# Performance work log

Hardware: AMD Instinct MI355X
Metric: run time of the kernel (lower is better)

Reference implementation:

```python
import jax, jax.numpy as jnp
import numpy as np


def setup_inputs() -> dict:
    key = jax.random.key(0)
    k1, k2 = jax.random.split(key)
    x = jax.random.normal(k1, (16, 256, 128, 128), dtype=jnp.float32)
    conv_w = jax.random.normal(k2, (1, 2, 3, 3), dtype=jnp.float32) * 0.1
    return {"x": x, "conv_w": conv_w}


def reference(x, conv_w):
    # x: [B, C, H, W]; channel-wise mean and max -> [B, 2, H, W]
    x_avg = jnp.mean(x, axis=1, keepdims=True)
    x_max = jnp.max(x, axis=1, keepdims=True)
    feat = jnp.concatenate([x_avg, x_max], axis=1)
    # 3x3 conv, stride 1, padding 1, no bias; NCHW / OIHW
    y = jax.lax.conv_general_dilated(
        feat, conv_w,
        window_strides=(1, 1), padding=((1, 1), (1, 1)),
        dimension_numbers=("NCHW", "OIHW", "NCHW"))
    return jax.nn.sigmoid(y)  # [B, 1, H, W]
```

## Files before the change

kernel.cpp:

```cpp
#include <hip/hip_runtime.h>
#include <math.h>

#define B 16
#define C 256
#define H 128
#define W 128
#define HW (H * W)
#define HW4 (HW / 4)

typedef float vfloat4 __attribute__((ext_vector_type(4)));

__global__ __launch_bounds__(256, 4) void reduce_mean_max(
    const float* __restrict__ x, float* __restrict__ feat) {
  const int t    = threadIdx.x;
  const int lane = t & 63;
  const int cq   = t >> 6;
  const int chunk = blockIdx.x * 64 + lane;
  const int b    = chunk >> 12;
  const int s4   = chunk & (HW4 - 1);

  const vfloat4* xp = (const vfloat4*)x + (size_t)(b * C + cq * 64) * HW4 + s4;

  vfloat4 sum = (vfloat4)(0.f);
  vfloat4 mx  = (vfloat4)(-INFINITY);
#pragma unroll 8
  for (int c = 0; c < 64; ++c) {
    vfloat4 v = xp[(size_t)c * HW4];
    sum += v;
    mx.x = fmaxf(mx.x, v.x); mx.y = fmaxf(mx.y, v.y);
    mx.z = fmaxf(mx.z, v.z); mx.w = fmaxf(mx.w, v.w);
  }

  __shared__ vfloat4 s_sum[4][64];
  __shared__ vfloat4 s_max[4][64];
  s_sum[cq][lane] = sum;
  s_max[cq][lane] = mx;
  __syncthreads();

  if (cq == 0) {
    vfloat4 a = s_sum[0][lane], b1 = s_sum[1][lane],
            c2 = s_sum[2][lane], d = s_sum[3][lane];
    const float inv = 1.0f / (float)C;
    vfloat4 mean = (a + b1 + c2 + d) * inv;
    ((vfloat4*)feat)[(size_t)(b * 2) * HW4 + s4] = mean;
  } else if (cq == 1) {
    vfloat4 a = s_max[0][lane], b1 = s_max[1][lane],
            c2 = s_max[2][lane], d = s_max[3][lane];
    vfloat4 m;
    m.x = fmaxf(fmaxf(a.x, b1.x), fmaxf(c2.x, d.x));
    m.y = fmaxf(fmaxf(a.y, b1.y), fmaxf(c2.y, d.y));
    m.z = fmaxf(fmaxf(a.z, b1.z), fmaxf(c2.z, d.z));
    m.w = fmaxf(fmaxf(a.w, b1.w), fmaxf(c2.w, d.w));
    ((vfloat4*)feat)[(size_t)(b * 2 + 1) * HW4 + s4] = m;
  }
}

__global__ __launch_bounds__(256) void conv3x3_sigmoid(
    const float* __restrict__ feat, const float* __restrict__ wgt,
    float* __restrict__ out) {
  __shared__ float sw[18];
  if (threadIdx.x < 18) sw[threadIdx.x] = wgt[threadIdx.x];
  __syncthreads();

  const int idx = blockIdx.x * 256 + threadIdx.x;
  const int b = idx >> 14;
  const int s = idx & (HW - 1);
  const int h = s >> 7;
  const int w = s & (W - 1);

  float acc = 0.f;
#pragma unroll
  for (int ci = 0; ci < 2; ++ci) {
    const float* f  = feat + (size_t)(b * 2 + ci) * HW;
    const float* kw = sw + ci * 9;
#pragma unroll
    for (int dh = -1; dh <= 1; ++dh) {
      const int hh = h + dh;
      if (hh < 0 || hh >= H) continue;
      const float* row = f + hh * W;
#pragma unroll
      for (int dw = -1; dw <= 1; ++dw) {
        const int ww = w + dw;
        if (ww < 0 || ww >= W) continue;
        acc += row[ww] * kw[(dh + 1) * 3 + (dw + 1)];
      }
    }
  }
  out[idx] = 1.f / (1.f + __expf(-acc));
}

extern "C" void kernel_launch(void* const* d_in, const int* in_sizes, int n_in,
                              void* d_out, int out_size, void* d_ws, size_t ws_size,
                              hipStream_t stream) {
  const float* x   = (const float*)d_in[0];
  const float* wgt = (const float*)d_in[1];
  float* out  = (float*)d_out;
  float* feat = (float*)d_ws;

  reduce_mean_max<<<1024, 256, 0, stream>>>(x, feat);
  conv3x3_sigmoid<<<1024, 256, 0, stream>>>(feat, wgt, out);
}
```

Measured before the change: 356.7 us.

## Restructure channel reduction into larger blocks with per-thread multi-chunk accumulation

The mean/max reduction now uses 256 blocks of 512 threads. Each wave handles 32 channels and each thread accumulates four separate spatial vectors, giving more independent loads in flight per thread. Partial results are combined across 8 waves through a shared buffer in two passes (sum, then max). This trades occupancy and block count for per-thread memory-level parallelism, and leaves exactly one block per CU.

```diff
diff --git a/kernel.cpp b/kernel.cpp
--- a/kernel.cpp
+++ b/kernel.cpp
@@ -10,48 +10,69 @@
 
 typedef float vfloat4 __attribute__((ext_vector_type(4)));
 
-__global__ __launch_bounds__(256, 4) void reduce_mean_max(
+__global__ __launch_bounds__(512) void reduce_mean_max(
     const float* __restrict__ x, float* __restrict__ feat) {
   const int t    = threadIdx.x;
   const int lane = t & 63;
-  const int cq   = t >> 6;
-  const int chunk = blockIdx.x * 64 + lane;
-  const int b    = chunk >> 12;
-  const int s4   = chunk & (HW4 - 1);
+  const int wv   = t >> 6;
+  const int sp   = blockIdx.x;
+  const int b    = sp >> 4;
+  const int s4b  = (sp & 15) << 8;
 
-  const vfloat4* xp = (const vfloat4*)x + (size_t)(b * C + cq * 64) * HW4 + s4;
+  const vfloat4* xp =
+      (const vfloat4*)x + (size_t)(b * C + wv * 32) * HW4 + s4b;
 
-  vfloat4 sum = (vfloat4)(0.f);
-  vfloat4 mx  = (vfloat4)(-INFINITY);
-#pragma unroll 8
-  for (int c = 0; c < 64; ++c) {
-    vfloat4 v = xp[(size_t)c * HW4];
-    sum += v;
-    mx.x = fmaxf(mx.x, v.x); mx.y = fmaxf(mx.y, v.y);
-    mx.z = fmaxf(mx.z, v.z); mx.w = fmaxf(mx.w, v.w);
+  vfloat4 sum[4], mx[4];
+#pragma unroll
+  for (int i = 0; i < 4; ++i) {
+    sum[i] = (vfloat4)(0.f);
+    mx[i]  = (vfloat4)(-INFINITY);
   }
 
-  __shared__ vfloat4 s_sum[4][64];
-  __shared__ vfloat4 s_max[4][64];
-  s_sum[cq][lane] = sum;
-  s_max[cq][lane] = mx;
+#pragma unroll 4
+  for (int c = 0; c < 32; ++c) {
+    const vfloat4* p = xp + (size_t)c * HW4;
+#pragma unroll
+    for (int i = 0; i < 4; ++i) {
+      vfloat4 v = p[i * 64 + lane];
+      sum[i] += v;
+      mx[i].x = fmaxf(mx[i].x, v.x);
+      mx[i].y = fmaxf(mx[i].y, v.y);
+      mx[i].z = fmaxf(mx[i].z, v.z);
+      mx[i].w = fmaxf(mx[i].w, v.w);
+    }
+  }
+
+  __shared__ vfloat4 s_buf[8][64][4];
+
+#pragma unroll
+  for (int i = 0; i < 4; ++i) s_buf[wv][lane][i] = sum[i];
+  __syncthreads();
+  if (t < 256) {
+    const int i = t >> 6, l = t & 63;
+    vfloat4 a = (vfloat4)(0.f);
+#pragma unroll
+    for (int w2 = 0; w2 < 8; ++w2) a += s_buf[w2][l][i];
+    const float inv = 1.0f / (float)C;
+    ((vfloat4*)feat)[(size_t)(b * 2) * HW4 + s4b + t] = a * inv;
+  }
   __syncthreads();
 
-  if (cq == 0) {
-    vfloat4 a = s_sum[0][lane], b1 = s_sum[1][lane],
-            c2 = s_sum[2][lane], d = s_sum[3][lane];
-    const float inv = 1.0f / (float)C;
-    vfloat4 mean = (a + b1 + c2 + d) * inv;
-    ((vfloat4*)feat)[(size_t)(b * 2) * HW4 + s4] = mean;
-  } else if (cq == 1) {
-    vfloat4 a = s_max[0][lane], b1 = s_max[1][lane],
-            c2 = s_max[2][lane], d = s_max[3][lane];
-    vfloat4 m;
-    m.x = fmaxf(fmaxf(a.x, b1.x), fmaxf(c2.x, d.x));
-    m.y = fmaxf(fmaxf(a.y, b1.y), fmaxf(c2.y, d.y));
-    m.z = fmaxf(fmaxf(a.z, b1.z), fmaxf(c2.z, d.z));
-    m.w = fmaxf(fmaxf(a.w, b1.w), fmaxf(c2.w, d.w));
-    ((vfloat4*)feat)[(size_t)(b * 2 + 1) * HW4 + s4] = m;
+#pragma unroll
+  for (int i = 0; i < 4; ++i) s_buf[wv][lane][i] = mx[i];
+  __syncthreads();
+  if (t < 256) {
+    const int i = t >> 6, l = t & 63;
+    vfloat4 m = s_buf[0][l][i];
+#pragma unroll
+    for (int w2 = 1; w2 < 8; ++w2) {
+      vfloat4 v = s_buf[w2][l][i];
+      m.x = fmaxf(m.x, v.x);
+      m.y = fmaxf(m.y, v.y);
+      m.z = fmaxf(m.z, v.z);
+      m.w = fmaxf(m.w, v.w);
+    }
+    ((vfloat4*)feat)[(size_t)(b * 2 + 1) * HW4 + s4b + t] = m;
   }
 }
 
@@ -97,6 +118,6 @@
   float* out  = (float*)d_out;
   float* feat = (float*)d_ws;
 
-  reduce_mean_max<<<1024, 256, 0, stream>>>(x, feat);
+  reduce_mean_max<<<256, 512, 0, stream>>>(x, feat);
   conv3x3_sigmoid<<<1024, 256, 0, stream>>>(feat, wgt, out);
 }
```

Result: no change. 353.8 us (-0.8%).
